# Kernel tuning notes

Hardware: AMD Instinct MI355X
Metric: run time of the kernel (lower is better)

## Reference

```python
import jax, jax.numpy as jnp
import numpy as np

B = 32          # batch size
N_IN = 1000000  # dofs of source function space (CG1 mesh)
N_OUT = 500000  # number of evaluation points (DG0 on VertexOnlyMesh)
K = 3           # nonzeros per row (CG1 barycentric interpolation)


def setup_inputs() -> dict:
    key = jax.random.key(0)
    k1, k2, k3 = jax.random.split(key, 3)
    x = jax.random.normal(k1, (B, N_IN), dtype=jnp.float32)
    # barycentric-style weights: nonnegative, rows sum to 1
    w_raw = jax.random.uniform(k2, (N_OUT, K), dtype=jnp.float32)
    w = w_raw / jnp.sum(w_raw, axis=1, keepdims=True)
    idx = jax.random.randint(k3, (N_OUT, K), 0, N_IN, dtype=jnp.int32)
    return {"x": x, "w": w, "idx": idx}


def reference(x, w, idx):
    # y = A @ x^T per sample, with A the sparse interpolation operator:
    # y[b, o] = sum_k w[o, k] * x[b, idx[o, k]]
    gathered = x[:, idx]                      # [B, N_OUT, K] gather
    return jnp.einsum("ok,bok->bo", w, gathered)  # [B, N_OUT]
```

## Files before the change

### kernel.cpp

```cpp
#include <hip/hip_runtime.h>
#include <hip/hip_bf16.h>

#define B_DIM 32
#define N_IN 1000000
#define N_OUT 500000

typedef float  nfloat4 __attribute__((ext_vector_type(4)));

__device__ __forceinline__ unsigned int f32_to_bf16_rne(float f) {
    unsigned int u = __float_as_uint(f);
    unsigned int rounding = 0x7fffu + ((u >> 16) & 1u);
    return (u + rounding) >> 16;
}

__global__ __launch_bounds__(256) void transpose_bf16_kernel(
    const float* __restrict__ x, unsigned short* __restrict__ xT)
{
    __shared__ unsigned int tile[64][17];
    const int t  = threadIdx.x;
    const int i0 = blockIdx.x * 64;

    const int qi = t & 15;
    const int p  = t >> 4;

    const float* r0 = x + (size_t)(2 * p)     * N_IN + i0 + qi * 4;
    const float* r1 = x + (size_t)(2 * p + 1) * N_IN + i0 + qi * 4;
    const nfloat4 va = __builtin_nontemporal_load((const nfloat4*)r0);
    const nfloat4 vb = __builtin_nontemporal_load((const nfloat4*)r1);

    tile[qi * 4 + 0][p] = f32_to_bf16_rne(va.x) | (f32_to_bf16_rne(vb.x) << 16);
    tile[qi * 4 + 1][p] = f32_to_bf16_rne(va.y) | (f32_to_bf16_rne(vb.y) << 16);
    tile[qi * 4 + 2][p] = f32_to_bf16_rne(va.z) | (f32_to_bf16_rne(vb.z) << 16);
    tile[qi * 4 + 3][p] = f32_to_bf16_rne(va.w) | (f32_to_bf16_rne(vb.w) << 16);
    __syncthreads();

    const int ii = t >> 2;
    const int g  = t & 3;
    uint4 pk;
    pk.x = tile[ii][g * 4 + 0];
    pk.y = tile[ii][g * 4 + 1];
    pk.z = tile[ii][g * 4 + 2];
    pk.w = tile[ii][g * 4 + 3];
    *(uint4*)((char*)xT + (size_t)(i0 + ii) * 64 + g * 16) = pk;
}

__global__ __launch_bounds__(256) void gather_bf16_kernel(
    const unsigned short* __restrict__ xT,
    const float* __restrict__ w,
    const int*   __restrict__ idx,
    float* __restrict__ out)
{
    const int o = blockIdx.x * blockDim.x + threadIdx.x;
    if (o >= N_OUT) return;

    const int base = 3 * o;
    const int i0 = idx[base + 0];
    const int i1 = idx[base + 1];
    const int i2 = idx[base + 2];
    const float w0 = w[base + 0];
    const float w1 = w[base + 1];
    const float w2 = w[base + 2];

    const uint4* __restrict__ p0 = (const uint4*)(xT + (size_t)i0 * B_DIM);
    const uint4* __restrict__ p1 = (const uint4*)(xT + (size_t)i1 * B_DIM);
    const uint4* __restrict__ p2 = (const uint4*)(xT + (size_t)i2 * B_DIM);

    uint4 v0[4], v1[4], v2[4];
#pragma unroll
    for (int q = 0; q < 4; ++q) v0[q] = p0[q];
#pragma unroll
    for (int q = 0; q < 4; ++q) v1[q] = p1[q];
#pragma unroll
    for (int q = 0; q < 4; ++q) v2[q] = p2[q];

    float acc[B_DIM];
#pragma unroll
    for (int b = 0; b < B_DIM; ++b) acc[b] = 0.0f;

#pragma unroll
    for (int q = 0; q < 4; ++q) {
        const unsigned int u0[4] = {v0[q].x, v0[q].y, v0[q].z, v0[q].w};
        const unsigned int u1[4] = {v1[q].x, v1[q].y, v1[q].z, v1[q].w};
        const unsigned int u2[4] = {v2[q].x, v2[q].y, v2[q].z, v2[q].w};
#pragma unroll
        for (int m = 0; m < 4; ++m) {
            const int b = q * 8 + m * 2;
            float a = acc[b], c = acc[b + 1];
            a = fmaf(w0, __uint_as_float(u0[m] << 16), a);
            c = fmaf(w0, __uint_as_float(u0[m] & 0xffff0000u), c);
            a = fmaf(w1, __uint_as_float(u1[m] << 16), a);
            c = fmaf(w1, __uint_as_float(u1[m] & 0xffff0000u), c);
            a = fmaf(w2, __uint_as_float(u2[m] << 16), a);
            c = fmaf(w2, __uint_as_float(u2[m] & 0xffff0000u), c);
            acc[b] = a; acc[b + 1] = c;
        }
    }

#pragma unroll
    for (int b = 0; b < B_DIM; ++b) {
        __builtin_nontemporal_store(acc[b], &out[(size_t)b * N_OUT + o]);
    }
}

__global__ __launch_bounds__(256) void direct_kernel(
    const float* __restrict__ x,
    const float* __restrict__ w,
    const int*   __restrict__ idx,
    float* __restrict__ out)
{
    const int o = blockIdx.x * blockDim.x + threadIdx.x;
    if (o >= N_OUT) return;
    const int base = 3 * o;
    const int i0 = idx[base + 0], i1 = idx[base + 1], i2 = idx[base + 2];
    const float w0 = w[base + 0], w1 = w[base + 1], w2 = w[base + 2];
#pragma unroll 4
    for (int b = 0; b < B_DIM; ++b) {
        const float* __restrict__ xr = x + (size_t)b * N_IN;
        float acc = w0 * xr[i0];
        acc = fmaf(w1, xr[i1], acc);
        acc = fmaf(w2, xr[i2], acc);
        out[(size_t)b * N_OUT + o] = acc;
    }
}

extern "C" void kernel_launch(void* const* d_in, const int* in_sizes, int n_in,
                              void* d_out, int out_size, void* d_ws, size_t ws_size,
                              hipStream_t stream) {
    const float* x   = (const float*)d_in[0];
    const float* w   = (const float*)d_in[1];
    const int*   idx = (const int*)d_in[2];
    float* out = (float*)d_out;

    const size_t xt_bytes = (size_t)N_IN * B_DIM * sizeof(unsigned short);

    if (ws_size >= xt_bytes) {
        unsigned short* xT = (unsigned short*)d_ws;
        transpose_bf16_kernel<<<N_IN / 64, 256, 0, stream>>>(x, xT);
        const int blocks = (N_OUT + 255) / 256;
        gather_bf16_kernel<<<blocks, 256, 0, stream>>>(xT, w, idx, out);
    } else {
        const int blocks = (N_OUT + 255) / 256;
        direct_kernel<<<blocks, 256, 0, stream>>>(x, w, idx, out);
    }
}
```

Before: 254.2 us.

## Split each output row across four threads in bf16 gather kernel

The gather kernel now assigns each output point to four cooperating lanes. Each lane loads one 16-byte quarter of the three 64-byte bf16 rows and computes 8 of the 32 batch outputs, instead of one thread loading all 192 bytes and computing all 32. This raises thread-level parallelism and memory coalescing per gathered row and cuts register pressure. The cost is four redundant loads of idx and w per output (now nontemporal) and output stores strided across four batch groups.

```diff
diff --git a/kernel.cpp b/kernel.cpp
--- a/kernel.cpp
+++ b/kernel.cpp
@@ -5,7 +5,7 @@
 #define N_IN 1000000
 #define N_OUT 500000
 
-typedef float  nfloat4 __attribute__((ext_vector_type(4)));
+typedef float nfloat4 __attribute__((ext_vector_type(4)));
 
 __device__ __forceinline__ unsigned int f32_to_bf16_rne(float f) {
     unsigned int u = __float_as_uint(f);
@@ -44,61 +44,53 @@
     *(uint4*)((char*)xT + (size_t)(i0 + ii) * 64 + g * 16) = pk;
 }
 
-__global__ __launch_bounds__(256) void gather_bf16_kernel(
+__global__ __launch_bounds__(256) void gather_bf16_v2_kernel(
     const unsigned short* __restrict__ xT,
     const float* __restrict__ w,
     const int*   __restrict__ idx,
     float* __restrict__ out)
 {
-    const int o = blockIdx.x * blockDim.x + threadIdx.x;
+    const int t = threadIdx.x;
+    const int g = t >> 2;
+    const int l = t & 3;
+    const int o = blockIdx.x * 64 + g;
     if (o >= N_OUT) return;
 
     const int base = 3 * o;
-    const int i0 = idx[base + 0];
-    const int i1 = idx[base + 1];
-    const int i2 = idx[base + 2];
-    const float w0 = w[base + 0];
-    const float w1 = w[base + 1];
-    const float w2 = w[base + 2];
+    const int   i0 = __builtin_nontemporal_load(idx + base + 0);
+    const int   i1 = __builtin_nontemporal_load(idx + base + 1);
+    const int   i2 = __builtin_nontemporal_load(idx + base + 2);
+    const float w0 = __builtin_nontemporal_load(w + base + 0);
+    const float w1 = __builtin_nontemporal_load(w + base + 1);
+    const float w2 = __builtin_nontemporal_load(w + base + 2);
 
-    const uint4* __restrict__ p0 = (const uint4*)(xT + (size_t)i0 * B_DIM);
-    const uint4* __restrict__ p1 = (const uint4*)(xT + (size_t)i1 * B_DIM);
-    const uint4* __restrict__ p2 = (const uint4*)(xT + (size_t)i2 * B_DIM);
+    const uint4 v0 = *(const uint4*)(xT + (size_t)i0 * B_DIM + l * 8);
+    const uint4 v1 = *(const uint4*)(xT + (size_t)i1 * B_DIM + l * 8);
+    const uint4 v2 = *(const uint4*)(xT + (size_t)i2 * B_DIM + l * 8);
 
-    uint4 v0[4], v1[4], v2[4];
+    float acc[8];
 #pragma unroll
-    for (int q = 0; q < 4; ++q) v0[q] = p0[q];
+    for (int j = 0; j < 8; ++j) acc[j] = 0.0f;
+
+    const unsigned int u0[4] = {v0.x, v0.y, v0.z, v0.w};
+    const unsigned int u1[4] = {v1.x, v1.y, v1.z, v1.w};
+    const unsigned int u2[4] = {v2.x, v2.y, v2.z, v2.w};
 #pragma unroll
-    for (int q = 0; q < 4; ++q) v1[q] = p1[q];
-#pragma unroll
-    for (int q = 0; q < 4; ++q) v2[q] = p2[q];
-
-    float acc[B_DIM];
-#pragma unroll
-    for (int b = 0; b < B_DIM; ++b) acc[b] = 0.0f;
-
-#pragma unroll
-    for (int q = 0; q < 4; ++q) {
-        const unsigned int u0[4] = {v0[q].x, v0[q].y, v0[q].z, v0[q].w};
-        const unsigned int u1[4] = {v1[q].x, v1[q].y, v1[q].z, v1[q].w};
-        const unsigned int u2[4] = {v2[q].x, v2[q].y, v2[q].z, v2[q].w};
-#pragma unroll
-        for (int m = 0; m < 4; ++m) {
-            const int b = q * 8 + m * 2;
-            float a = acc[b], c = acc[b + 1];
-            a = fmaf(w0, __uint_as_float(u0[m] << 16), a);
-            c = fmaf(w0, __uint_as_float(u0[m] & 0xffff0000u), c);
-            a = fmaf(w1, __uint_as_float(u1[m] << 16), a);
-            c = fmaf(w1, __uint_as_float(u1[m] & 0xffff0000u), c);
-            a = fmaf(w2, __uint_as_float(u2[m] << 16), a);
-            c = fmaf(w2, __uint_as_float(u2[m] & 0xffff0000u), c);
-            acc[b] = a; acc[b + 1] = c;
-        }
+    for (int m = 0; m < 4; ++m) {
+        float a = acc[2 * m], c = acc[2 * m + 1];
+        a = fmaf(w0, __uint_as_float(u0[m] << 16), a);
+        c = fmaf(w0, __uint_as_float(u0[m] & 0xffff0000u), c);
+        a = fmaf(w1, __uint_as_float(u1[m] << 16), a);
+        c = fmaf(w1, __uint_as_float(u1[m] & 0xffff0000u), c);
+        a = fmaf(w2, __uint_as_float(u2[m] << 16), a);
+        c = fmaf(w2, __uint_as_float(u2[m] & 0xffff0000u), c);
+        acc[2 * m] = a; acc[2 * m + 1] = c;
     }
 
+    float* obase = out + (size_t)(8 * l) * N_OUT + o;
 #pragma unroll
-    for (int b = 0; b < B_DIM; ++b) {
-        __builtin_nontemporal_store(acc[b], &out[(size_t)b * N_OUT + o]);
+    for (int j = 0; j < 8; ++j) {
+        __builtin_nontemporal_store(acc[j], obase + (size_t)j * N_OUT);
     }
 }
 
@@ -136,8 +128,8 @@
     if (ws_size >= xt_bytes) {
         unsigned short* xT = (unsigned short*)d_ws;
         transpose_bf16_kernel<<<N_IN / 64, 256, 0, stream>>>(x, xT);
-        const int blocks = (N_OUT + 255) / 256;
-        gather_bf16_kernel<<<blocks, 256, 0, stream>>>(xT, w, idx, out);
+        const int blocks = (N_OUT + 63) / 64;
+        gather_bf16_v2_kernel<<<blocks, 256, 0, stream>>>(xT, w, idx, out);
     } else {
         const int blocks = (N_OUT + 255) / 256;
         direct_kernel<<<blocks, 256, 0, stream>>>(x, w, idx, out);
```

Measured after the change: 248.3 us. 1.02x faster.
